# Kernel optimization log

Measured on AMD Instinct MI355X. Metric: run time of the kernel, lower is better.

The kernel has to match this reference:

```python
import jax, jax.numpy as jnp
import numpy as np

B, T = 128, 100
DZ, DA, DU, K, DOBS, H = 64, 32, 8, 8, 16, 128
JITTER = 1e-4  # _safe_cholesky: sym + jitter*I, then first try adds 1.0*jitter*I again


def setup_inputs() -> dict:
    key = jax.random.key(0)
    ks = jax.random.split(key, 10)
    eye_z = jnp.eye(DZ, dtype=jnp.float32)
    # stable-ish per-component transition matrices
    A_mats = 0.9 * eye_z[None] + 0.05 * jax.random.normal(ks[0], (K, DZ, DZ), jnp.float32)
    B_mats = 0.1 * jax.random.normal(ks[1], (K, DZ, DU), jnp.float32)
    C_mats = 0.3 * jax.random.normal(ks[2], (K, DA, DZ), jnp.float32)
    a_seq = jax.random.normal(ks[3], (B, T, DA), jnp.float32)
    h_obs = jax.random.normal(ks[4], (B, DOBS), jnp.float32)
    u_seq = jax.random.normal(ks[5], (B, T, DU), jnp.float32)
    mask = jnp.ones((B, T), jnp.float32)
    a_0 = jnp.zeros((1, DA), jnp.float32)          # nn.Parameter a_0
    P_0 = 10.0 * eye_z                              # 10 * eye(dim_z)
    Q = 0.05 * eye_z                                # Q_std * eye(dim_z)
    R = 0.05 * jnp.eye(DA, dtype=jnp.float32)       # R_std * eye(dim_a)
    din = DA + DOBS + DU
    s = 1.0 / float(np.sqrt(H))
    W_ih = s * jax.random.normal(ks[6], (3 * H, din), jnp.float32)
    W_hh = s * jax.random.normal(ks[7], (3 * H, H), jnp.float32)
    b_ih = jnp.zeros((3 * H,), jnp.float32)
    b_hh = jnp.zeros((3 * H,), jnp.float32)
    W_out = s * jax.random.normal(ks[8], (K, H), jnp.float32)
    b_out = jnp.zeros((K,), jnp.float32)
    return dict(a_seq=a_seq, h_obs=h_obs, u_seq=u_seq, mask=mask,
                A_mats=A_mats, B_mats=B_mats, C_mats=C_mats,
                a_0=a_0, P_0=P_0, Q=Q, R=R,
                W_ih=W_ih, W_hh=W_hh, b_ih=b_ih, b_hh=b_hh,
                W_out=W_out, b_out=b_out, epoch=100)


def _sym(M):
    return 0.5 * (M + jnp.swapaxes(M, -1, -2))


def _gru_alpha(x, h, W_ih, W_hh, b_ih, b_hh, W_out, b_out):
    # GRU-cell alpha_net: mixture weights over K components
    gi = x @ W_ih.T + b_ih
    gh = h @ W_hh.T + b_hh
    ir, iz, inn = jnp.split(gi, 3, axis=-1)
    hr, hz, hn = jnp.split(gh, 3, axis=-1)
    r = jax.nn.sigmoid(ir + hr)
    zg = jax.nn.sigmoid(iz + hz)
    n = jnp.tanh(inn + r * hn)
    h_new = (1.0 - zg) * n + zg * h
    alpha = jax.nn.softmax(h_new @ W_out.T + b_out, axis=-1)
    return alpha, h_new


def _kalman_forward(a_seq, h_obs, u_seq, mask, A_mats, B_mats, C_mats,
                    a_0, P_0, Q, R, W_ih, W_hh, b_ih, b_hh, W_out, b_out):
    Bsz = a_seq.shape[0]
    I = jnp.eye(DZ, dtype=a_seq.dtype)

    def mix(alpha):
        A = jnp.einsum('bk,kij->bij', alpha, A_mats)
        Bc = jnp.einsum('bk,kij->bij', alpha, B_mats)
        C = jnp.einsum('bk,kij->bij', alpha, C_mats)
        return A, Bc, C

    def alpha_net(a, u, h):
        x = jnp.concatenate([a, h_obs, u], axis=-1)
        return _gru_alpha(x, h, W_ih, W_hh, b_ih, b_hh, W_out, b_out)

    gru_h = jnp.zeros((Bsz, H), a_seq.dtype)
    a_prev = jnp.broadcast_to(a_0, (Bsz, DA))
    alpha0, gru_h = alpha_net(a_prev, u_seq[:, 0], gru_h)
    A_k0, B_k0, C_k0 = mix(alpha0)

    z0 = jnp.zeros((Bsz, DZ), a_seq.dtype)
    P0 = jnp.broadcast_to(P_0, (Bsz, DZ, DZ))

    def step(carry, inp):
        z_prev, P, h, A_k, B_k, C_k = carry
        a_k, u_k, m_k = inp  # [B,da], [B,du], [B]
        mk = m_k[:, None]
        # predict with matrices chosen at previous step
        z = jnp.einsum('bij,bj->bi', A_k, z_prev) + jnp.einsum('bij,bj->bi', B_k, u_k)
        a_hat = jnp.einsum('bij,bj->bi', C_k, z)
        r_k = a_k - a_hat
        CP = jnp.einsum('bij,bjk->bik', C_k, P)                      # C P
        S = jnp.einsum('bik,bjk->bij', CP, C_k) + R                   # C P C^T + R
        # K = solve(S^T, C P^T)^T  (i.e. K = P C^T S^{-1})
        CPt = jnp.einsum('bij,bkj->bik', C_k, P)
        Kg = jnp.swapaxes(jnp.linalg.solve(jnp.swapaxes(S, -1, -2), CPt), -1, -2)
        Kg = Kg * m_k[:, None, None]
        IKC = I - jnp.einsum('bij,bjk->bik', Kg, C_k)
        # Joseph form update
        P_filt = (jnp.einsum('bij,bjk,blk->bil', IKC, P, IKC)
                  + jnp.einsum('bij,jk,blk->bil', Kg, R, Kg))
        P_filt = _sym(P_filt)
        z_mean = z + jnp.einsum('bij,bj->bi', Kg, r_k)
        L = jnp.linalg.cholesky(_sym(P_filt) + 2.0 * JITTER * I)      # safe cholesky
        z_filt = z_mean                                               # dist.mean
        a_filt = jnp.einsum('bij,bj->bi', C_k, z_filt)
        a_k_hat = mk * a_k + (1.0 - mk) * a_filt
        C_old = C_k
        alpha, h = alpha_net(a_k_hat, u_k, h)
        A_n, B_n, C_n = mix(alpha)
        z_pred = (jnp.einsum('bij,bj->bi', A_n, z_filt)
                  + jnp.einsum('bij,bj->bi', B_n, u_k))
        a_pred = jnp.einsum('bij,bj->bi', C_n, z_pred)
        P_pred = _sym(jnp.einsum('bij,bjk,blk->bil', A_n, P_filt, A_n) + Q)
        carry = (z_filt, P_pred, h, A_n, B_n, C_n)
        out = (z_filt, P_filt, z_pred, P_pred, alpha, a_filt, a_pred,
               S, z_mean, L, A_n, B_n, C_old)
        return carry, out

    xs = (jnp.swapaxes(a_seq, 0, 1), jnp.swapaxes(u_seq, 0, 1), jnp.swapaxes(mask, 0, 1))
    _, outs = jax.lax.scan(step, (z0, P0, gru_h, A_k0, B_k0, C_k0), xs)
    # scan outputs are [T, B, ...] -> [B, T, ...]
    (z_filt, P_filt, z_pred, P_pred, alpha_seq, a_filt, a_pred,
     S_pred, z_means, z_scale_tril, A_seq, B_seq, C_seq) = jax.tree.map(
        lambda x: jnp.swapaxes(x, 0, 1), outs)
    return (z_filt, P_filt, z_pred, a_filt, a_pred, P_pred, alpha_seq,
            A_seq, B_seq, C_seq, z_means, z_scale_tril, S_pred)


def reference(a_seq, h_obs, u_seq, mask, A_mats, B_mats, C_mats,
              a_0, P_0, Q, R, W_ih, W_hh, b_ih, b_hh, W_out, b_out, epoch):
    # epoch >= warmup/burn-in thresholds (all 0), so no detach branches apply
    return _kalman_forward(a_seq, h_obs, u_seq, mask, A_mats, B_mats, C_mats,
                           a_0, P_0, Q, R, W_ih, W_hh, b_ih, b_hh, W_out, b_out)
```

## Files before the change

### kernel.cpp

```cpp
#include <hip/hip_runtime.h>

typedef float f4 __attribute__((ext_vector_type(4)));

#define NT 256
#define BB 128
#define BT 100
#define DZc 64
#define DAc 32
#define DUc 8
#define KMIX 8
#define DOBSc 16
#define HG 128
#define DINc 56

#define O_ZFILT   0LL
#define O_PFILT   819200LL
#define O_ZPRED   53248000LL
#define O_AFILT   54067200LL
#define O_APRED   54476800LL
#define O_PPRED   54886400LL
#define O_ALPHA   107315200LL
#define O_ASEQ    107417600LL
#define O_BSEQ    159846400LL
#define O_CSEQ    166400000LL
#define O_ZMEAN   192614400LL
#define O_LTRIL   193433600LL
#define O_SPRED   245862400LL

__device__ __forceinline__ float dot4(f4 a, f4 b) {
    return a[0]*b[0] + a[1]*b[1] + a[2]*b[2] + a[3]*b[3];
}

struct SMem {
    float P[DZc][68];
    float A[DZc][68];
    float AT[DZc][68];
    float Wk[DZc][68];
    float Qm[DZc][68];
    float C[DAc][68];
    float CP[DAc][68];
    float Xm[DAc][68];
    float S[DAc][33];
    float Rm[DAc][33];
    float dinv[DAc];
    float Bm[DZc][8];
    float z[DZc], zp[DZc], zn[DZc];
    float h[HG];
    float gh[3*HG], gi[3*HG];
    float x[64];
    float ak[DAc], rvec[DAc];
    float u[8];
    float lg[8];
    float mk;
};

template<bool EMIT>
__device__ __forceinline__ void mix_apply(SMem& s, int tid, size_t bt, const float* al8,
    const float* __restrict__ A_mats, const float* __restrict__ B_mats,
    const float* __restrict__ C_mats, float* __restrict__ out)
{
    const f4* A4 = (const f4*)A_mats;
    const f4* B4 = (const f4*)B_mats;
    const f4* C4 = (const f4*)C_mats;
    #pragma unroll 2
    for (int e = 0; e < 4; ++e) {
        int i4 = tid + e*256;
        f4 acc = {0.f,0.f,0.f,0.f};
        #pragma unroll
        for (int k = 0; k < 8; ++k) acc += al8[k] * A4[k*1024 + i4];
        int row = i4 >> 4, cb = (i4 & 15) * 4;
        *(f4*)&s.A[row][cb] = acc;
        s.AT[cb][row] = acc[0]; s.AT[cb+1][row] = acc[1];
        s.AT[cb+2][row] = acc[2]; s.AT[cb+3][row] = acc[3];
        if (EMIT) *(f4*)&out[O_ASEQ + bt*4096 + (size_t)i4*4] = acc;
    }
    if (tid < 128) {
        int i4 = tid;
        f4 acc = {0.f,0.f,0.f,0.f};
        #pragma unroll
        for (int k = 0; k < 8; ++k) acc += al8[k] * B4[k*128 + i4];
        *(f4*)&s.Bm[i4>>1][(i4&1)*4] = acc;
        if (EMIT) *(f4*)&out[O_BSEQ + bt*512 + (size_t)i4*4] = acc;
    }
    #pragma unroll 1
    for (int e = 0; e < 2; ++e) {
        int i4 = tid + e*256;
        f4 acc = {0.f,0.f,0.f,0.f};
        #pragma unroll
        for (int k = 0; k < 8; ++k) acc += al8[k] * C4[k*512 + i4];
        *(f4*)&s.C[i4>>4][(i4&15)*4] = acc;
    }
}

__global__ void __launch_bounds__(NT, 1)
kalman_seq(const float* __restrict__ a_seq, const float* __restrict__ h_obs,
           const float* __restrict__ u_seq, const float* __restrict__ mask,
           const float* __restrict__ A_mats, const float* __restrict__ B_mats,
           const float* __restrict__ C_mats, const float* __restrict__ a_0,
           const float* __restrict__ P_0, const float* __restrict__ Q,
           const float* __restrict__ R, const float* __restrict__ W_ih,
           const float* __restrict__ W_hh, const float* __restrict__ b_ih,
           const float* __restrict__ b_hh, const float* __restrict__ W_out,
           const float* __restrict__ b_out, float* __restrict__ out)
{
    __shared__ SMem s;
    const int b = blockIdx.x;
    const int tid = threadIdx.x;
    const int r4 = (tid >> 4) << 2;
    const int c4 = (tid & 15) << 2;

    for (int idx = tid; idx < DZc*DZc; idx += NT) {
        s.P[idx >> 6][idx & 63]  = P_0[idx];
        s.Qm[idx >> 6][idx & 63] = Q[idx];
    }
    for (int idx = tid; idx < DAc*DAc; idx += NT) s.Rm[idx >> 5][idx & 31] = R[idx];
    if (tid < HG) s.h[tid] = 0.f;
    if (tid < DZc) s.z[tid] = 0.f;
    if (tid < DAc)                 s.x[tid] = a_0[tid];
    else if (tid < DAc + DOBSc)    s.x[tid] = h_obs[b*DOBSc + (tid - DAc)];
    else if (tid < DINc)           s.x[tid] = u_seq[(size_t)b*BT*DUc + (tid - DAc - DOBSc)];
    __syncthreads();

    for (int g = tid; g < 3*HG; g += NT) {
        const float* wi = W_ih + (size_t)g * DINc;
        f4 ai = {0.f,0.f,0.f,0.f};
        #pragma unroll 7
        for (int q = 0; q < 14; ++q) ai += *(const f4*)(wi + q*4) * *(const f4*)&s.x[q*4];
        s.gi[g] = ai[0]+ai[1]+ai[2]+ai[3] + b_ih[g];
        s.gh[g] = b_hh[g];
    }
    __syncthreads();
    if (tid < HG) {
        float r  = 1.f / (1.f + expf(-(s.gi[tid] + s.gh[tid])));
        float zg = 1.f / (1.f + expf(-(s.gi[HG+tid] + s.gh[HG+tid])));
        float n  = tanhf(s.gi[2*HG+tid] + r * s.gh[2*HG+tid]);
        s.h[tid] = (1.f - zg) * n;
    }
    __syncthreads();
    if (tid < KMIX) {
        const float* wo = W_out + tid * HG;
        f4 acc = {0.f,0.f,0.f,0.f};
        #pragma unroll 8
        for (int q = 0; q < 32; ++q) acc += *(const f4*)(wo + q*4) * *(const f4*)&s.h[q*4];
        s.lg[tid] = acc[0]+acc[1]+acc[2]+acc[3] + b_out[tid];
    }
    __syncthreads();
    {
        float lg[8];
        #pragma unroll
        for (int k = 0; k < 8; ++k) lg[k] = s.lg[k];
        float mx = lg[0];
        #pragma unroll
        for (int k = 1; k < 8; ++k) mx = fmaxf(mx, lg[k]);
        float al[8]; float sum = 0.f;
        #pragma unroll
        for (int k = 0; k < 8; ++k) { al[k] = expf(lg[k] - mx); sum += al[k]; }
        float rs = 1.f / sum;
        #pragma unroll
        for (int k = 0; k < 8; ++k) al[k] *= rs;
        mix_apply<false>(s, tid, 0, al, A_mats, B_mats, C_mats, out);
    }
    __syncthreads();

    for (int t = 0; t < BT; ++t) {
        const size_t bt = (size_t)b * BT + t;

        if (tid < 64) {
            float acc = 0.f;
            #pragma unroll 8
            for (int k = 0; k < DZc; ++k) acc += s.AT[k][tid] * s.z[k];
            const float* up = u_seq + bt*DUc;
            #pragma unroll
            for (int q = 0; q < DUc; ++q) acc += s.Bm[tid][q] * up[q];
            s.zp[tid] = acc;
        } else if (tid < 96) {
            float av = a_seq[bt*DAc + (tid-64)];
            s.ak[tid-64] = av;
            s.x[tid-64] = av;
        } else if (tid < 104) {
            float uv = u_seq[bt*DUc + (tid-96)];
            s.u[tid-96] = uv; s.x[48 + (tid-96)] = uv;
        } else if (tid == 104) {
            s.mk = mask[bt];
        }
        __syncthreads();
        const float mkv = s.mk;
        const bool mk1 = (mkv == 1.0f);

        {
            const int r = tid >> 3;
            const int c8 = (tid & 7) * 8;
            f4 acc0 = {0.f,0.f,0.f,0.f}, acc1 = {0.f,0.f,0.f,0.f};
            #pragma unroll 4
            for (int k4 = 0; k4 < 16; ++k4) {
                f4 cr = *(const f4*)&s.C[r][k4*4];
                #pragma unroll
                for (int kk = 0; kk < 4; ++kk) {
                    float cv = cr[kk];
                    acc0 += cv * *(const f4*)&s.P[k4*4+kk][c8];
                    acc1 += cv * *(const f4*)&s.P[k4*4+kk][c8+4];
                }
            }
            *(f4*)&s.CP[r][c8]   = acc0;
            *(f4*)&s.CP[r][c8+4] = acc1;
        }
        if (tid < DAc) {
            float acc = 0.f;
            #pragma unroll 4
            for (int k4 = 0; k4 < 16; ++k4)
                acc += dot4(*(const f4*)&s.C[tid][k4*4], *(const f4*)&s.zp[k4*4]);
            s.rvec[tid] = s.ak[tid] - acc;
        }
        __syncthreads();

        {
            const int r = tid >> 3;
            const int cb = (tid & 7) * 4;
            f4 acc = {0.f,0.f,0.f,0.f};
            #pragma unroll 4
            for (int k4 = 0; k4 < 16; ++k4) {
                f4 a = *(const f4*)&s.CP[r][k4*4];
                #pragma unroll
                for (int j = 0; j < 4; ++j)
                    acc[j] += dot4(a, *(const f4*)&s.C[cb+j][k4*4]);
            }
            f4 rm = {s.Rm[r][cb], s.Rm[r][cb+1], s.Rm[r][cb+2], s.Rm[r][cb+3]};
            f4 v = acc + rm;
            s.S[r][cb] = v[0]; s.S[r][cb+1] = v[1]; s.S[r][cb+2] = v[2]; s.S[r][cb+3] = v[3];
            *(f4*)&out[O_SPRED + bt*1024 + (size_t)r*32 + cb] = v;
        }
        __syncthreads();

        if (tid < 64) {
            const int lane = tid;
            const int l = lane & 31, par = lane >> 5;
            for (int k = 0; k < 31; ++k) {
                __threadfence_block();
                float dv = 1.0f / s.S[k][k];
                if (lane == k) s.dinv[k] = dv;
                if (l > k) {
                    float f = s.S[l][k] * dv;
                    for (int j = k + 1 + par; j <= l; j += 2)
                        s.S[l][j] -= f * s.S[j][k];
                }
            }
            __threadfence_block();
            if (lane == 31) s.dinv[31] = 1.0f / s.S[31][31];
            __threadfence_block();
            #pragma unroll 8
            for (int r = 0; r < 32; ++r) s.Xm[r][lane] = s.CP[r][lane];
            s.Xm[0][lane] *= s.dinv[0];
            #pragma unroll 1
            for (int r = 1; r < 32; ++r) {
                float acc = s.Xm[r][lane];
                #pragma unroll 4
                for (int k = 0; k < r; ++k) acc -= s.S[r][k] * s.Xm[k][lane];
                s.Xm[r][lane] = s.dinv[r] * acc;
            }
            #pragma unroll 1
            for (int r = 30; r >= 0; --r) {
                float acc = 0.f;
                #pragma unroll 4
                for (int k = r+1; k < 32; ++k) acc += s.S[k][r] * s.Xm[k][lane];
                s.Xm[r][lane] -= s.dinv[r] * acc;
            }
            float accz = 0.f;
            #pragma unroll 4
            for (int r = 0; r < 32; ++r) accz += s.Xm[r][lane] * s.rvec[r];
            s.zn[lane] = s.zp[lane] + mkv * accz;
        } else {
            #pragma unroll 1
            for (int g = tid - 64; g < 3*HG; g += 192) {
                const float* wi = W_ih + (size_t)g * DINc;
                const float* wh = W_hh + (size_t)g * HG;
                f4 ai = {0.f,0.f,0.f,0.f}, ah = {0.f,0.f,0.f,0.f};
                #pragma unroll 7
                for (int q = 0; q < 14; ++q) ai += *(const f4*)(wi + q*4) * *(const f4*)&s.x[q*4];
                #pragma unroll 8
                for (int q = 0; q < 32; ++q) ah += *(const f4*)(wh + q*4) * *(const f4*)&s.h[q*4];
                s.gi[g] = ai[0]+ai[1]+ai[2]+ai[3] + b_ih[g];
                s.gh[g] = ah[0]+ah[1]+ah[2]+ah[3] + b_hh[g];
            }
        }
        __syncthreads();

        {
            const float coef = (mkv*mkv - 2.f*mkv) * 0.5f;
            f4 acc0 = {0.f,0.f,0.f,0.f}, acc1 = {0.f,0.f,0.f,0.f};
            f4 acc2 = {0.f,0.f,0.f,0.f}, acc3 = {0.f,0.f,0.f,0.f};
            #pragma unroll 4
            for (int l = 0; l < DAc; ++l) {
                f4 cpc = *(const f4*)&s.CP[l][c4];
                f4 xc  = *(const f4*)&s.Xm[l][c4];
                f4 cpr = *(const f4*)&s.CP[l][r4];
                f4 xr  = *(const f4*)&s.Xm[l][r4];
                acc0 += xr[0]*cpc + cpr[0]*xc;
                acc1 += xr[1]*cpc + cpr[1]*xc;
                acc2 += xr[2]*cpc + cpr[2]*xc;
                acc3 += xr[3]*cpc + cpr[3]*xc;
            }
            #pragma unroll
            for (int i = 0; i < 4; ++i) {
                const int row = r4 + i;
                f4 g = (i==0) ? acc0 : (i==1) ? acc1 : (i==2) ? acc2 : acc3;
                f4 p = *(const f4*)&s.P[row][c4];
                f4 v = p + coef * g;
                *(f4*)&s.P[row][c4] = v;
                *(f4*)&out[O_PFILT + bt*4096 + (size_t)row*64 + c4] = v;
            }
        }
        if (tid < DZc) {
            float v = s.zn[tid];
            out[O_ZFILT + bt*DZc + tid] = v;
            out[O_ZMEAN + bt*DZc + tid] = v;
            s.z[tid] = v;
        }
        if (tid < DAc) {
            float acc = 0.f;
            #pragma unroll 4
            for (int k4 = 0; k4 < 16; ++k4)
                acc += dot4(*(const f4*)&s.C[tid][k4*4], *(const f4*)&s.zn[k4*4]);
            out[O_AFILT + bt*DAc + tid] = acc;
            s.x[tid] = mkv * s.ak[tid] + (1.f - mkv) * acc;
        }
        #pragma unroll 1
        for (int e = 0; e < 2; ++e) {
            int i4 = tid + e*256;
            *(f4*)&out[O_CSEQ + bt*2048 + (size_t)i4*4] = *(const f4*)&s.C[i4>>4][(i4&15)*4];
        }
        if (mk1 && tid < HG) {
            float gi0 = s.gi[tid], gi1 = s.gi[HG+tid], gi2 = s.gi[2*HG+tid];
            float gh0 = s.gh[tid], gh1 = s.gh[HG+tid], gh2 = s.gh[2*HG+tid];
            float hold = s.h[tid];
            float r  = 1.f / (1.f + expf(-(gi0 + gh0)));
            float zg = 1.f / (1.f + expf(-(gi1 + gh1)));
            float n  = tanhf(gi2 + r * gh2);
            s.h[tid] = (1.f - zg) * n + zg * hold;
        }
        __syncthreads();

        if (!mk1) {
            for (int g = tid; g < 3*HG; g += NT) {
                const float* wi = W_ih + (size_t)g * DINc;
                f4 ai = {0.f,0.f,0.f,0.f};
                #pragma unroll 7
                for (int q = 0; q < 14; ++q) ai += *(const f4*)(wi + q*4) * *(const f4*)&s.x[q*4];
                s.gi[g] = ai[0]+ai[1]+ai[2]+ai[3] + b_ih[g];
            }
            __syncthreads();
            if (tid < HG) {
                float gi0 = s.gi[tid], gi1 = s.gi[HG+tid], gi2 = s.gi[2*HG+tid];
                float gh0 = s.gh[tid], gh1 = s.gh[HG+tid], gh2 = s.gh[2*HG+tid];
                float hold = s.h[tid];
                float r  = 1.f / (1.f + expf(-(gi0 + gh0)));
                float zg = 1.f / (1.f + expf(-(gi1 + gh1)));
                float n  = tanhf(gi2 + r * gh2);
                s.h[tid] = (1.f - zg) * n + zg * hold;
            }
            __syncthreads();
        }

        if (tid < KMIX) {
            const float* wo = W_out + tid * HG;
            f4 acc = {0.f,0.f,0.f,0.f};
            #pragma unroll 8
            for (int q = 0; q < 32; ++q) acc += *(const f4*)(wo + q*4) * *(const f4*)&s.h[q*4];
            s.lg[tid] = acc[0]+acc[1]+acc[2]+acc[3] + b_out[tid];
        }
        __syncthreads();

        {
            float lg[8];
            #pragma unroll
            for (int k = 0; k < 8; ++k) lg[k] = s.lg[k];
            float mx = lg[0];
            #pragma unroll
            for (int k = 1; k < 8; ++k) mx = fmaxf(mx, lg[k]);
            float al[8]; float sum = 0.f;
            #pragma unroll
            for (int k = 0; k < 8; ++k) { al[k] = expf(lg[k] - mx); sum += al[k]; }
            float rs = 1.f / sum;
            #pragma unroll
            for (int k = 0; k < 8; ++k) al[k] *= rs;
            if (tid < 8) out[O_ALPHA + bt*8 + tid] = al[tid];
            mix_apply<true>(s, tid, bt, al, A_mats, B_mats, C_mats, out);
        }
        __syncthreads();

        if (tid < DZc) {
            float acc = 0.f;
            #pragma unroll 4
            for (int k4 = 0; k4 < 16; ++k4)
                acc += dot4(*(const f4*)&s.A[tid][k4*4], *(const f4*)&s.z[k4*4]);
            acc += dot4(*(const f4*)&s.Bm[tid][0], *(const f4*)&s.u[0]);
            acc += dot4(*(const f4*)&s.Bm[tid][4], *(const f4*)&s.u[4]);
            s.zp[tid] = acc;
            out[O_ZPRED + bt*DZc + tid] = acc;
        }
        {
            f4 acc[4] = {{0.f,0.f,0.f,0.f},{0.f,0.f,0.f,0.f},{0.f,0.f,0.f,0.f},{0.f,0.f,0.f,0.f}};
            #pragma unroll 2
            for (int k4 = 0; k4 < 16; ++k4) {
                #pragma unroll
                for (int kk = 0; kk < 4; ++kk) {
                    f4 bv = *(const f4*)&s.P[k4*4+kk][c4];
                    #pragma unroll
                    for (int i = 0; i < 4; ++i)
                        acc[i] += s.A[r4+i][k4*4+kk] * bv;
                }
            }
            #pragma unroll
            for (int i = 0; i < 4; ++i)
                *(f4*)&s.Wk[r4+i][c4] = acc[i];
        }
        __syncthreads();

        {
            f4 acc[4] = {{0.f,0.f,0.f,0.f},{0.f,0.f,0.f,0.f},{0.f,0.f,0.f,0.f},{0.f,0.f,0.f,0.f}};
            #pragma unroll 2
            for (int k4 = 0; k4 < 16; ++k4) {
                #pragma unroll
                for (int kk = 0; kk < 4; ++kk) {
                    f4 av = *(const f4*)&s.AT[k4*4+kk][c4];
                    #pragma unroll
                    for (int i = 0; i < 4; ++i)
                        acc[i] += s.Wk[r4+i][k4*4+kk] * av;
                }
            }
            #pragma unroll
            for (int i = 0; i < 4; ++i) {
                const int row = r4 + i;
                f4 q = *(const f4*)&s.Qm[row][c4];
                f4 v = acc[i] + q;
                *(f4*)&s.P[row][c4] = v;
                *(f4*)&out[O_PPRED + bt*4096 + (size_t)row*64 + c4] = v;
            }
        }
        if (tid < DAc) {
            float acc = 0.f;
            #pragma unroll 4
            for (int k4 = 0; k4 < 16; ++k4)
                acc += dot4(*(const f4*)&s.C[tid][k4*4], *(const f4*)&s.zp[k4*4]);
            out[O_APRED + bt*DAc + tid] = acc;
        }
        __syncthreads();
    }
}

__global__ void __launch_bounds__(64)
chol_batch(float* __restrict__ out)
{
    __shared__ float M[DZc][65];
    __shared__ float sd[DZc];
    const size_t bt = blockIdx.x;
    const int lane = threadIdx.x;
    const float* src = out + O_PFILT + bt*4096;
    #pragma unroll 4
    for (int e = 0; e < 16; ++e) {
        int i4 = lane + e*64;
        f4 v = *(const f4*)(src + (size_t)i4*4);
        int row = i4 >> 4, cb = (i4 & 15) * 4;
        M[row][cb] = v[0]; M[row][cb+1] = v[1]; M[row][cb+2] = v[2]; M[row][cb+3] = v[3];
    }
    __syncthreads();
    M[lane][lane] += 2.0e-4f;
    __syncthreads();
    for (int k = 0; k < DZc; ++k) {
        __threadfence_block();
        float mkk = M[k][k];
        if (lane == k) sd[k] = sqrtf(mkk);
        if (lane > k) {
            float f = M[lane][k] / mkk;
            for (int j = k + 1; j <= lane; ++j)
                M[lane][j] -= f * M[j][k];
        }
    }
    __threadfence_block();
    for (int k = 0; k < lane; ++k) M[lane][k] /= sd[k];
    M[lane][lane] = sd[lane];
    for (int k = lane + 1; k < DZc; ++k) M[lane][k] = 0.f;
    __syncthreads();
    float* dst = out + O_LTRIL + bt*4096;
    #pragma unroll 4
    for (int e = 0; e < 16; ++e) {
        int i4 = lane + e*64;
        int row = i4 >> 4, cb = (i4 & 15) * 4;
        f4 v = {M[row][cb], M[row][cb+1], M[row][cb+2], M[row][cb+3]};
        *(f4*)(dst + (size_t)i4*4) = v;
    }
}

extern "C" void kernel_launch(void* const* d_in, const int* in_sizes, int n_in,
                              void* d_out, int out_size, void* d_ws, size_t ws_size,
                              hipStream_t stream) {
    const float* a_seq  = (const float*)d_in[0];
    const float* h_obs  = (const float*)d_in[1];
    const float* u_seq  = (const float*)d_in[2];
    const float* mask   = (const float*)d_in[3];
    const float* A_mats = (const float*)d_in[4];
    const float* B_mats = (const float*)d_in[5];
    const float* C_mats = (const float*)d_in[6];
    const float* a_0    = (const float*)d_in[7];
    const float* P_0    = (const float*)d_in[8];
    const float* Q      = (const float*)d_in[9];
    const float* R      = (const float*)d_in[10];
    const float* W_ih   = (const float*)d_in[11];
    const float* W_hh   = (const float*)d_in[12];
    const float* b_ih   = (const float*)d_in[13];
    const float* b_hh   = (const float*)d_in[14];
    const float* W_out  = (const float*)d_in[15];
    const float* b_out  = (const float*)d_in[16];
    float* out = (float*)d_out;

    kalman_seq<<<dim3(BB), dim3(NT), 0, stream>>>(a_seq, h_obs, u_seq, mask,
        A_mats, B_mats, C_mats, a_0, P_0, Q, R, W_ih, W_hh, b_ih, b_hh, W_out, b_out, out);
    chol_batch<<<dim3(BB*BT), dim3(64), 0, stream>>>(out);
}
```

Measured before the change: 7.501 ms.

## Fuse GRU update into solve phase and drop per-step barriers

Each of 128 threads now computes all three GRU gates for one hidden unit, including the nonlinearity, and writes to a new double-buffered hidden state. This overlaps with the triangular solve done by the first wavefront, which keeps the solve in registers and also computes a_filt itself. Idle threads write C_seq during that phase, and the W_out logits are computed with wave shuffles, removing several __syncthreads per timestep. The A·P and W·A^T loops load rows as f4 vectors. In exchange there is heavier register use (a 32-float array plus six accumulators) and more serial work per GRU thread.

```diff
diff --git a/kernel.cpp b/kernel.cpp
--- a/kernel.cpp
+++ b/kernel.cpp
@@ -45,7 +45,7 @@
     float dinv[DAc];
     float Bm[DZc][8];
     float z[DZc], zp[DZc], zn[DZc];
-    float h[HG];
+    float h[HG], hn[HG];
     float gh[3*HG], gi[3*HG];
     float x[64];
     float ak[DAc], rvec[DAc];
@@ -247,39 +247,79 @@
             __threadfence_block();
             if (lane == 31) s.dinv[31] = 1.0f / s.S[31][31];
             __threadfence_block();
-            #pragma unroll 8
-            for (int r = 0; r < 32; ++r) s.Xm[r][lane] = s.CP[r][lane];
-            s.Xm[0][lane] *= s.dinv[0];
-            #pragma unroll 1
-            for (int r = 1; r < 32; ++r) {
-                float acc = s.Xm[r][lane];
-                #pragma unroll 4
-                for (int k = 0; k < r; ++k) acc -= s.S[r][k] * s.Xm[k][lane];
-                s.Xm[r][lane] = s.dinv[r] * acc;
-            }
-            #pragma unroll 1
+            float v[32];
+            #pragma unroll
+            for (int r = 0; r < 32; ++r) v[r] = s.CP[r][lane];
+            #pragma unroll
+            for (int r = 0; r < 32; ++r) {
+                float acc = v[r];
+                #pragma unroll
+                for (int k = 0; k < r; ++k) acc -= s.S[r][k] * v[k];
+                v[r] = s.dinv[r] * acc;
+            }
+            #pragma unroll
             for (int r = 30; r >= 0; --r) {
                 float acc = 0.f;
+                #pragma unroll
+                for (int k = r+1; k < 32; ++k) acc += s.S[k][r] * v[k];
+                v[r] -= s.dinv[r] * acc;
+            }
+            float accz = 0.f;
+            #pragma unroll
+            for (int r = 0; r < 32; ++r) {
+                s.Xm[r][lane] = v[r];
+                accz += v[r] * s.rvec[r];
+            }
+            s.zn[lane] = s.zp[lane] + mkv * accz;
+            __threadfence_block();
+            if (lane < DAc) {
+                float acc = 0.f;
                 #pragma unroll 4
-                for (int k = r+1; k < 32; ++k) acc += s.S[k][r] * s.Xm[k][lane];
-                s.Xm[r][lane] -= s.dinv[r] * acc;
-            }
-            float accz = 0.f;
-            #pragma unroll 4
-            for (int r = 0; r < 32; ++r) accz += s.Xm[r][lane] * s.rvec[r];
-            s.zn[lane] = s.zp[lane] + mkv * accz;
+                for (int k4 = 0; k4 < 16; ++k4)
+                    acc += dot4(*(const f4*)&s.C[lane][k4*4], *(const f4*)&s.zn[k4*4]);
+                out[O_AFILT + bt*DAc + lane] = acc;
+                if (!mk1) s.x[lane] = mkv * s.ak[lane] + (1.f - mkv) * acc;
+            }
+        } else if (tid < 192) {
+            const int idx = tid - 64;
+            const float* wir = W_ih + (size_t)idx * DINc;
+            const float* wiz = W_ih + (size_t)(HG + idx) * DINc;
+            const float* win = W_ih + (size_t)(2*HG + idx) * DINc;
+            const float* whr = W_hh + (size_t)idx * HG;
+            const float* whz = W_hh + (size_t)(HG + idx) * HG;
+            const float* whn = W_hh + (size_t)(2*HG + idx) * HG;
+            f4 air = {0.f,0.f,0.f,0.f}, aiz = {0.f,0.f,0.f,0.f}, ain = {0.f,0.f,0.f,0.f};
+            #pragma unroll 7
+            for (int q = 0; q < 14; ++q) {
+                f4 xv = *(const f4*)&s.x[q*4];
+                air += *(const f4*)(wir + q*4) * xv;
+                aiz += *(const f4*)(wiz + q*4) * xv;
+                ain += *(const f4*)(win + q*4) * xv;
+            }
+            f4 ahr = {0.f,0.f,0.f,0.f}, ahz = {0.f,0.f,0.f,0.f}, ahn = {0.f,0.f,0.f,0.f};
+            #pragma unroll 8
+            for (int q = 0; q < 32; ++q) {
+                f4 hv = *(const f4*)&s.h[q*4];
+                ahr += *(const f4*)(whr + q*4) * hv;
+                ahz += *(const f4*)(whz + q*4) * hv;
+                ahn += *(const f4*)(whn + q*4) * hv;
+            }
+            float gir = air[0]+air[1]+air[2]+air[3] + b_ih[idx];
+            float giz = aiz[0]+aiz[1]+aiz[2]+aiz[3] + b_ih[HG + idx];
+            float gin = ain[0]+ain[1]+ain[2]+ain[3] + b_ih[2*HG + idx];
+            float ghr = ahr[0]+ahr[1]+ahr[2]+ahr[3] + b_hh[idx];
+            float ghz = ahz[0]+ahz[1]+ahz[2]+ahz[3] + b_hh[HG + idx];
+            float ghn = ahn[0]+ahn[1]+ahn[2]+ahn[3] + b_hh[2*HG + idx];
+            float r  = 1.f / (1.f + expf(-(gir + ghr)));
+            float zg = 1.f / (1.f + expf(-(giz + ghz)));
+            float n  = tanhf(gin + r * ghn);
+            s.hn[idx] = (1.f - zg) * n + zg * s.h[idx];
         } else {
-            #pragma unroll 1
-            for (int g = tid - 64; g < 3*HG; g += 192) {
-                const float* wi = W_ih + (size_t)g * DINc;
-                const float* wh = W_hh + (size_t)g * HG;
-                f4 ai = {0.f,0.f,0.f,0.f}, ah = {0.f,0.f,0.f,0.f};
-                #pragma unroll 7
-                for (int q = 0; q < 14; ++q) ai += *(const f4*)(wi + q*4) * *(const f4*)&s.x[q*4];
-                #pragma unroll 8
-                for (int q = 0; q < 32; ++q) ah += *(const f4*)(wh + q*4) * *(const f4*)&s.h[q*4];
-                s.gi[g] = ai[0]+ai[1]+ai[2]+ai[3] + b_ih[g];
-                s.gh[g] = ah[0]+ah[1]+ah[2]+ah[3] + b_hh[g];
+            const int l = tid - 192;
+            #pragma unroll 2
+            for (int e = 0; e < 8; ++e) {
+                int i4 = l + e*64;
+                *(f4*)&out[O_CSEQ + bt*2048 + (size_t)i4*4] = *(const f4*)&s.C[i4>>4][(i4&15)*4];
             }
         }
         __syncthreads();
@@ -315,37 +355,19 @@
             out[O_ZMEAN + bt*DZc + tid] = v;
             s.z[tid] = v;
         }
-        if (tid < DAc) {
-            float acc = 0.f;
-            #pragma unroll 4
-            for (int k4 = 0; k4 < 16; ++k4)
-                acc += dot4(*(const f4*)&s.C[tid][k4*4], *(const f4*)&s.zn[k4*4]);
-            out[O_AFILT + bt*DAc + tid] = acc;
-            s.x[tid] = mkv * s.ak[tid] + (1.f - mkv) * acc;
-        }
-        #pragma unroll 1
-        for (int e = 0; e < 2; ++e) {
-            int i4 = tid + e*256;
-            *(f4*)&out[O_CSEQ + bt*2048 + (size_t)i4*4] = *(const f4*)&s.C[i4>>4][(i4&15)*4];
-        }
-        if (mk1 && tid < HG) {
-            float gi0 = s.gi[tid], gi1 = s.gi[HG+tid], gi2 = s.gi[2*HG+tid];
-            float gh0 = s.gh[tid], gh1 = s.gh[HG+tid], gh2 = s.gh[2*HG+tid];
-            float hold = s.h[tid];
-            float r  = 1.f / (1.f + expf(-(gi0 + gh0)));
-            float zg = 1.f / (1.f + expf(-(gi1 + gh1)));
-            float n  = tanhf(gi2 + r * gh2);
-            s.h[tid] = (1.f - zg) * n + zg * hold;
-        }
-        __syncthreads();
 
         if (!mk1) {
+            __syncthreads();
             for (int g = tid; g < 3*HG; g += NT) {
                 const float* wi = W_ih + (size_t)g * DINc;
-                f4 ai = {0.f,0.f,0.f,0.f};
+                const float* wh = W_hh + (size_t)g * HG;
+                f4 ai = {0.f,0.f,0.f,0.f}, ah = {0.f,0.f,0.f,0.f};
                 #pragma unroll 7
                 for (int q = 0; q < 14; ++q) ai += *(const f4*)(wi + q*4) * *(const f4*)&s.x[q*4];
+                #pragma unroll 8
+                for (int q = 0; q < 32; ++q) ah += *(const f4*)(wh + q*4) * *(const f4*)&s.h[q*4];
                 s.gi[g] = ai[0]+ai[1]+ai[2]+ai[3] + b_ih[g];
+                s.gh[g] = ah[0]+ah[1]+ah[2]+ah[3] + b_hh[g];
             }
             __syncthreads();
             if (tid < HG) {
@@ -355,24 +377,24 @@
                 float r  = 1.f / (1.f + expf(-(gi0 + gh0)));
                 float zg = 1.f / (1.f + expf(-(gi1 + gh1)));
                 float n  = tanhf(gi2 + r * gh2);
-                s.h[tid] = (1.f - zg) * n + zg * hold;
+                s.hn[tid] = (1.f - zg) * n + zg * hold;
             }
             __syncthreads();
         }
 
-        if (tid < KMIX) {
-            const float* wo = W_out + tid * HG;
-            f4 acc = {0.f,0.f,0.f,0.f};
-            #pragma unroll 8
-            for (int q = 0; q < 32; ++q) acc += *(const f4*)(wo + q*4) * *(const f4*)&s.h[q*4];
-            s.lg[tid] = acc[0]+acc[1]+acc[2]+acc[3] + b_out[tid];
-        }
-        __syncthreads();
-
         {
+            const int lane = tid & 63;
+            const int g = lane >> 3;
+            const int cb = (lane & 7) * 16;
+            f4 a4 = {0.f,0.f,0.f,0.f};
+            #pragma unroll
+            for (int q = 0; q < 4; ++q)
+                a4 += *(const f4*)(W_out + (size_t)g*HG + cb + q*4) * *(const f4*)&s.hn[cb + q*4];
+            float acc = a4[0]+a4[1]+a4[2]+a4[3];
+            acc += __shfl_xor(acc, 1); acc += __shfl_xor(acc, 2); acc += __shfl_xor(acc, 4);
             float lg[8];
             #pragma unroll
-            for (int k = 0; k < 8; ++k) lg[k] = s.lg[k];
+            for (int k = 0; k < 8; ++k) lg[k] = __shfl(acc, k*8) + b_out[k];
             float mx = lg[0];
             #pragma unroll
             for (int k = 1; k < 8; ++k) mx = fmaxf(mx, lg[k]);
@@ -385,13 +407,13 @@
             if (tid < 8) out[O_ALPHA + bt*8 + tid] = al[tid];
             mix_apply<true>(s, tid, bt, al, A_mats, B_mats, C_mats, out);
         }
-        __syncthreads();
-
-        if (tid < DZc) {
+        if (tid < HG) s.h[tid] = s.hn[tid];
+        __syncthreads();
+
+        if (tid < 64) {
             float acc = 0.f;
-            #pragma unroll 4
-            for (int k4 = 0; k4 < 16; ++k4)
-                acc += dot4(*(const f4*)&s.A[tid][k4*4], *(const f4*)&s.z[k4*4]);
+            #pragma unroll 8
+            for (int k = 0; k < DZc; ++k) acc += s.AT[k][tid] * s.z[k];
             acc += dot4(*(const f4*)&s.Bm[tid][0], *(const f4*)&s.u[0]);
             acc += dot4(*(const f4*)&s.Bm[tid][4], *(const f4*)&s.u[4]);
             s.zp[tid] = acc;
@@ -401,12 +423,15 @@
             f4 acc[4] = {{0.f,0.f,0.f,0.f},{0.f,0.f,0.f,0.f},{0.f,0.f,0.f,0.f},{0.f,0.f,0.f,0.f}};
             #pragma unroll 2
             for (int k4 = 0; k4 < 16; ++k4) {
+                f4 ar0 = *(const f4*)&s.A[r4+0][k4*4];
+                f4 ar1 = *(const f4*)&s.A[r4+1][k4*4];
+                f4 ar2 = *(const f4*)&s.A[r4+2][k4*4];
+                f4 ar3 = *(const f4*)&s.A[r4+3][k4*4];
                 #pragma unroll
                 for (int kk = 0; kk < 4; ++kk) {
                     f4 bv = *(const f4*)&s.P[k4*4+kk][c4];
-                    #pragma unroll
-                    for (int i = 0; i < 4; ++i)
-                        acc[i] += s.A[r4+i][k4*4+kk] * bv;
+                    acc[0] += ar0[kk] * bv; acc[1] += ar1[kk] * bv;
+                    acc[2] += ar2[kk] * bv; acc[3] += ar3[kk] * bv;
                 }
             }
             #pragma unroll
@@ -419,12 +444,15 @@
             f4 acc[4] = {{0.f,0.f,0.f,0.f},{0.f,0.f,0.f,0.f},{0.f,0.f,0.f,0.f},{0.f,0.f,0.f,0.f}};
             #pragma unroll 2
             for (int k4 = 0; k4 < 16; ++k4) {
+                f4 w0 = *(const f4*)&s.Wk[r4+0][k4*4];
+                f4 w1 = *(const f4*)&s.Wk[r4+1][k4*4];
+                f4 w2 = *(const f4*)&s.Wk[r4+2][k4*4];
+                f4 w3 = *(const f4*)&s.Wk[r4+3][k4*4];
                 #pragma unroll
                 for (int kk = 0; kk < 4; ++kk) {
                     f4 av = *(const f4*)&s.AT[k4*4+kk][c4];
-                    #pragma unroll
-                    for (int i = 0; i < 4; ++i)
-                        acc[i] += s.Wk[r4+i][k4*4+kk] * av;
+                    acc[0] += w0[kk] * av; acc[1] += w1[kk] * av;
+                    acc[2] += w2[kk] * av; acc[3] += w3[kk] * av;
                 }
             }
             #pragma unroll
```

Measured after the change: 7.302 ms. 2.7% less time.
